# Kernel optimization log

Hardware: AMD Instinct MI355X
Metric: run time of the kernel (lower is better)

Reference implementation:

```python
import jax, jax.numpy as jnp
import numpy as np

C = 64; NET = 32; K = 3; G = 4; GC = C // G; P = K * K
STRIDE = 1; PAD = 1; DIL = 1; OFFSET_SCALE = 1.0
BN_EPS = 1e-5; LN_EPS = 1e-6


def conv2d(x, w, b, groups=1, pad=1):
    # x: (N,C,H,W), w: (O, I//groups, kh, kw)
    y = jax.lax.conv_general_dilated(
        x, w, (1, 1), [(pad, pad), (pad, pad)],
        feature_group_count=groups,
        dimension_numbers=('NCHW', 'OIHW', 'NCHW'))
    return y + b[None, :, None, None]


def dcnv3_core(x, offset, mask):
    """Faithful port of dcnv3_core_pytorch (InternImage).
    x: (N,H,W,C) channels-last; offset: (N,H,W,G*P*2); mask: (N,H,W,G*P) (softmaxed).
    grid_sample(bilinear, zeros padding, align_corners=False) done manually."""
    xp = jnp.pad(x, ((0, 0), (PAD, PAD), (PAD, PAD), (0, 0)))
    N, Hin, Win, _ = xp.shape
    Ho, Wo = offset.shape[1], offset.shape[2]
    # reference points in normalized [0,1] coords (x first, y second)
    start = (DIL * (K - 1)) // 2 + 0.5
    ref_x = (start + jnp.arange(Wo, dtype=jnp.float32) * STRIDE) / Win  # (Wo,)
    ref_y = (start + jnp.arange(Ho, dtype=jnp.float32) * STRIDE) / Hin  # (Ho,)
    ref = jnp.stack(jnp.broadcast_arrays(ref_x[None, :], ref_y[:, None]), axis=-1)  # (Ho,Wo,2)
    # dilation grid (kernel tap offsets, torch meshgrid 'ij' flatten order: w-major)
    kv = (jnp.arange(K, dtype=jnp.float32) * DIL - (DIL * (K - 1)) // 2)
    gx, gy = jnp.meshgrid(kv / Win, kv / Hin, indexing='ij')
    grid = jnp.stack([gx, gy], -1).reshape(P, 2)  # (P,2), same for every group
    # sampling locations, normalized: (N,Ho,Wo,G,P,2)
    off = offset.reshape(N, Ho, Wo, G, P, 2) * (OFFSET_SCALE / jnp.array([Win, Hin], jnp.float32))
    loc = ref[None, :, :, None, None, :] + grid[None, None, None, None, :, :] * OFFSET_SCALE + off
    # grid_sample align_corners=False: pixel = loc*size - 0.5  (since g = 2*loc-1)
    px = loc[..., 0] * Win - 0.5
    py = loc[..., 1] * Hin - 0.5
    x0 = jnp.floor(px); y0 = jnp.floor(py)
    ix0 = x0.astype(jnp.int32); iy0 = y0.astype(jnp.int32)
    wx1 = px - x0; wy1 = py - y0; wx0 = 1.0 - wx1; wy0 = 1.0 - wy1
    xg = xp.reshape(N, Hin, Win, G, GC)
    n_idx = jnp.arange(N)[:, None, None, None, None]
    g_idx = jnp.arange(G)[None, None, None, :, None]

    def sample(ix, iy):
        valid = ((ix >= 0) & (ix < Win) & (iy >= 0) & (iy < Hin)).astype(xg.dtype)
        v = xg[n_idx, jnp.clip(iy, 0, Hin - 1), jnp.clip(ix, 0, Win - 1), g_idx]  # (N,Ho,Wo,G,P,GC)
        return v * valid[..., None]

    val = (sample(ix0, iy0) * (wx0 * wy0)[..., None]
           + sample(ix0 + 1, iy0) * (wx1 * wy0)[..., None]
           + sample(ix0, iy0 + 1) * (wx0 * wy1)[..., None]
           + sample(ix0 + 1, iy0 + 1) * (wx1 * wy1)[..., None])
    out = jnp.einsum('nhwgpc,nhwgp->nhwgc', val, mask.reshape(N, Ho, Wo, G, P))
    return out.reshape(N, Ho, Wo, C)


def setup_inputs() -> dict:
    key = jax.random.key(0)
    ks = jax.random.split(key, 16)
    N, H, W = 4, 128, 128
    f = lambda k, shp, s=1.0: jax.random.normal(k, shp, jnp.float32) * s
    return {
        'input_x': f(ks[0], (N, C, H, W)),
        'input_y': f(ks[1], (N, NET, H, W)),
        'enc_w': f(ks[2], (NET, C), 0.05), 'enc_b': jnp.zeros((NET,), jnp.float32),
        'bn_g': jnp.ones((NET,), jnp.float32), 'bn_b': jnp.zeros((NET,), jnp.float32),
        'bn_m': jnp.zeros((NET,), jnp.float32), 'bn_v': jnp.ones((NET,), jnp.float32),
        'gru_wz': f(ks[3], (NET, 2 * NET, 3, 3), 0.05), 'gru_bz': jnp.zeros((NET,), jnp.float32),
        'gru_wr': f(ks[4], (NET, 2 * NET, 3, 3), 0.05), 'gru_br': jnp.zeros((NET,), jnp.float32),
        'gru_wq': f(ks[5], (NET, 2 * NET, 3, 3), 0.05), 'gru_bq': jnp.zeros((NET,), jnp.float32),
        'dw_w': f(ks[6], (C, 1, 3, 3), 0.1), 'dw_b': jnp.zeros((C,), jnp.float32),
        'ln_g': jnp.ones((C,), jnp.float32), 'ln_b': jnp.zeros((C,), jnp.float32),
        'off_w': f(ks[7], (G * P * 2, C), 0.1), 'off_b': f(ks[8], (G * P * 2,), 0.1),
        'mask_w': f(ks[9], (G * P, C), 0.1), 'mask_b': jnp.zeros((G * P,), jnp.float32),
        'inp_w': f(ks[10], (C, C), 0.1), 'inp_b': jnp.zeros((C,), jnp.float32),
        'out_w': f(ks[11], (C, C), 0.1), 'out_b': jnp.zeros((C,), jnp.float32),
    }


def reference(input_x, input_y, enc_w, enc_b, bn_g, bn_b, bn_m, bn_v,
              gru_wz, gru_bz, gru_wr, gru_br, gru_wq, gru_bq,
              dw_w, dw_b, ln_g, ln_b, off_w, off_b, mask_w, mask_b,
              inp_w, inp_b, out_w, out_b):
    N, _, H, W = input_x.shape
    # encoder: 1x1 Conv + BN(eval) + SiLU
    e = jnp.einsum('nchw,oc->nohw', input_x, enc_w) + enc_b[None, :, None, None]
    e = (e - bn_m[None, :, None, None]) * jax.lax.rsqrt(bn_v + BN_EPS)[None, :, None, None]
    e = e * bn_g[None, :, None, None] + bn_b[None, :, None, None]
    x_en = jax.nn.silu(e)
    # ConvGRU: h' = (1-z)*h + z*q
    hx = jnp.concatenate([input_y, x_en], axis=1)
    z = jax.nn.sigmoid(conv2d(hx, gru_wz, gru_bz))
    r = jax.nn.sigmoid(conv2d(hx, gru_wr, gru_br))
    q = jnp.tanh(conv2d(jnp.concatenate([r * input_y, x_en], axis=1), gru_wq, gru_bq))
    h = (1.0 - z) * input_y + z * q  # (N,NET,H,W)
    # channels-last main path
    inp = input_x.transpose(0, 2, 3, 1)  # (N,H,W,C)
    x = inp @ inp_w.T + inp_b
    # depthwise conv on gru state -> LN (channels_last) -> GELU
    y = conv2d(h, dw_w, dw_b, groups=NET).transpose(0, 2, 3, 1)  # (N,H,W,C)
    mu = y.mean(-1, keepdims=True)
    var = ((y - mu) ** 2).mean(-1, keepdims=True)
    y = (y - mu) * jax.lax.rsqrt(var + LN_EPS) * ln_g + ln_b
    y = jax.nn.gelu(y, approximate=False)
    offset = y @ off_w.T + off_b  # (N,H,W,G*P*2)
    m = y @ mask_w.T + mask_b
    m = jax.nn.softmax(m.reshape(N, H, W, G, P), axis=-1).reshape(N, H, W, G * P)
    x = dcnv3_core(x, offset, m)
    x = x @ out_w.T + out_b
    return jax.nn.silu(x.transpose(0, 3, 1, 2)), h
```

## Files before the change

### kernel.cpp

```cpp
#include <hip/hip_runtime.h>
#include <hip/hip_bf16.h>

typedef __hip_bfloat16 bf16;
typedef short short8v __attribute__((ext_vector_type(8)));
typedef short short4v __attribute__((ext_vector_type(4)));
typedef float float4v __attribute__((ext_vector_type(4)));

static __device__ __forceinline__ float b2f(bf16 v){ return __bfloat162float(v); }
static __device__ __forceinline__ bf16 f2b(float v){ return __float2bfloat16(v); }
static __device__ __forceinline__ float bu2f(unsigned short u){ return __uint_as_float(((unsigned)u) << 16); }
static __device__ __forceinline__ short f2bs(float v){ bf16 t = __float2bfloat16(v); return *(short*)&t; }

#define WT 128
#define HWT 16384

#define OFF_ENC   0
#define OFF_ENCSC 2048
#define OFF_ENCSH 2080
#define OFF_BZ    20544
#define OFF_BR    39008
#define OFF_BQ    57472
#define OFF_DWP   57504
#define OFF_DWB   58080
#define OFF_LNG   58144
#define OFF_LNB   58208
#define OFF_OMB   65184
#define OFF_WINP  65296
#define OFF_BINP  69392
#define OFF_BOUT  73552
#define NW_TOTAL  73616
#define NBF_ZR    36864
#define NBF_Q     18432
#define NBF_OM    7168
#define NBF_OUT   4096
#define NPREP     (NW_TOTAL + NBF_ZR + NBF_Q + NBF_OM + NBF_OUT)
#define NHALO     2064
#define NTOT      (NPREP + NHALO)

#define B_WZRB  294912
#define B_WQB   368640
#define B_WOMB  405504
#define B_WOUTB 419840
#define B_HXP   428544
#define B_QINP  9081344
#define B_ZBUF  17734144
#define B_XL    428544

__global__ void k_prep(
    const float* __restrict__ enc_w, const float* __restrict__ enc_b,
    const float* __restrict__ bn_g, const float* __restrict__ bn_b,
    const float* __restrict__ bn_m, const float* __restrict__ bn_v,
    const float* __restrict__ gwz, const float* __restrict__ gbz,
    const float* __restrict__ gwr, const float* __restrict__ gbr,
    const float* __restrict__ gwq, const float* __restrict__ gbq,
    const float* __restrict__ dww, const float* __restrict__ dwb,
    const float* __restrict__ lng, const float* __restrict__ lnb,
    const float* __restrict__ offw, const float* __restrict__ offb,
    const float* __restrict__ maskw, const float* __restrict__ maskb,
    const float* __restrict__ inpw, const float* __restrict__ inpb,
    const float* __restrict__ outw, const float* __restrict__ outb,
    float* __restrict__ Wp, bf16* __restrict__ wzrb, bf16* __restrict__ wqb,
    bf16* __restrict__ womb, bf16* __restrict__ woutb,
    bf16* __restrict__ hxp, bf16* __restrict__ qinp) {
  int i = blockIdx.x * blockDim.x + threadIdx.x;
  if (i >= NTOT) return;
  if (i >= NPREP) {
    int t = i - NPREP;
    int img = t / 516, r = t % 516;
    int ph, pw;
    if (r < 130) { ph = 0; pw = r; }
    else if (r < 260) { ph = 129; pw = r - 130; }
    else if (r < 388) { ph = r - 260 + 1; pw = 0; }
    else { ph = r - 388 + 1; pw = 129; }
    size_t pb = (((size_t)img * 130 + ph) * 130 + pw) * 64;
    uint4 zz = make_uint4(0, 0, 0, 0);
    #pragma unroll
    for (int k = 0; k < 8; ++k) {
      ((uint4*)(hxp + pb))[k] = zz;
      ((uint4*)(qinp + pb))[k] = zz;
    }
    return;
  }
  if (i >= NW_TOTAL) {
    int d = i - NW_TOTAL;
    if (d < NBF_ZR) {
      int n = d / 576, k = d % 576;
      int tap = k >> 6, cin = k & 63;
      float v = (n < 32) ? gwz[(n*64 + cin)*9 + tap] : gwr[((n-32)*64 + cin)*9 + tap];
      wzrb[d] = f2b(v);
    } else if (d < NBF_ZR + NBF_Q) {
      int d2 = d - NBF_ZR;
      int n = d2 / 576, k = d2 % 576;
      int tap = k >> 6, cin = k & 63;
      wqb[d2] = f2b(gwq[(n*64 + cin)*9 + tap]);
    } else if (d < NBF_ZR + NBF_Q + NBF_OM) {
      int d3 = d - NBF_ZR - NBF_Q;
      int j = d3 >> 6, c = d3 & 63;
      float v = (j < 72) ? offw[j*64 + c] : ((j < 108) ? maskw[(j-72)*64 + c] : 0.f);
      womb[d3] = f2b(v);
    } else {
      int d4 = d - NBF_ZR - NBF_Q - NBF_OM;
      int o = d4 >> 6, c = d4 & 63;
      woutb[d4] = f2b(outw[o*64 + c]);
    }
    return;
  }
  float v;
  if (i < 2048) { int c = i >> 5, o = i & 31; v = enc_w[o*64 + c]; }
  else if (i < 2080) { int o = i - 2048; v = bn_g[o] * rsqrtf(bn_v[o] + 1e-5f); }
  else if (i < 2112) { int o = i - 2080;
    float sc = bn_g[o] * rsqrtf(bn_v[o] + 1e-5f);
    v = (enc_b[o] - bn_m[o]) * sc + bn_b[o]; }
  else if (i < 20544) { v = 0.f; }
  else if (i < 20576) { v = gbz[i - OFF_BZ]; }
  else if (i < 39008) { v = 0.f; }
  else if (i < 39040) { v = gbr[i - OFF_BR]; }
  else if (i < 57472) { v = 0.f; }
  else if (i < 57504) { v = gbq[i - OFF_BQ]; }
  else if (i < 58080) { int d = i - OFF_DWP; int tap = d >> 6, o = d & 63; v = dww[o*9 + tap]; }
  else if (i < 58144) { v = dwb[i - OFF_DWB]; }
  else if (i < 58208) { v = lng[i - OFF_LNG]; }
  else if (i < 58272) { v = lnb[i - OFF_LNB]; }
  else if (i < 65184) { v = 0.f; }
  else if (i < 65292) { int j = i - OFF_OMB; v = (j < 72) ? offb[j] : maskb[j-72]; }
  else if (i < 65296) { v = 0.f; }
  else if (i < 69392) { int d = i - OFF_WINP; int c = d >> 6, o = d & 63; v = inpw[o*64 + c]; }
  else if (i < 69456) { v = inpb[i - OFF_BINP]; }
  else if (i < 73552) { v = 0.f; }
  else { v = outb[i - OFF_BOUT]; }
  Wp[i] = v;
}

__global__ void __launch_bounds__(256) k_pre(
    const float* __restrict__ X, const float* __restrict__ Y,
    const float* __restrict__ Wp, bf16* __restrict__ hxp, bf16* __restrict__ qinp) {
  __shared__ float xls[4096];
  int tid = threadIdx.x;
  int px = tid & 63, sect = tid >> 6;
  int img = blockIdx.z, h = blockIdx.y, w0 = blockIdx.x * 64;
  int hw = h * WT + w0 + px;
  const float* xp = X + (size_t)img * (64 * HWT) + hw;
  #pragma unroll
  for (int i = 0; i < 16; ++i) {
    int c = sect * 16 + i;
    xls[c * 64 + px] = xp[c * HWT];
  }
  const float* yp = Y + (size_t)img * (32 * HWT) + hw;
  bf16 yv[8];
  #pragma unroll
  for (int i = 0; i < 8; ++i) yv[i] = f2b(yp[(sect * 8 + i) * HWT]);
  size_t pb = (((size_t)img * 130 + h + 1) * 130 + (w0 + px + 1)) * 64;
  *(uint4*)(hxp + pb + sect * 8) = *(const uint4*)yv;
  __syncthreads();
  float aen[8];
  #pragma unroll
  for (int o = 0; o < 8; ++o) aen[o] = 0.f;
  for (int k = 0; k < 64; ++k) {
    float a = xls[k * 64 + px];
    const float* we = Wp + OFF_ENC + k * 32 + sect * 8;
    #pragma unroll
    for (int o = 0; o < 8; ++o) aen[o] += a * we[o];
  }
  bf16 xe[8];
  #pragma unroll
  for (int o = 0; o < 8; ++o) {
    int oo = sect * 8 + o;
    float e = aen[o] * Wp[OFF_ENCSC + oo] + Wp[OFF_ENCSH + oo];
    xe[o] = f2b(e / (1.f + __expf(-e)));
  }
  *(uint4*)(hxp + pb + 32 + sect * 8) = *(const uint4*)xe;
  *(uint4*)(qinp + pb + 32 + sect * 8) = *(const uint4*)xe;
}

__global__ void __launch_bounds__(256) k_zr(
    const float* __restrict__ Wp,
    const bf16* __restrict__ hxp, const bf16* __restrict__ wzrb,
    bf16* __restrict__ qinp, bf16* __restrict__ zbuf) {
  __shared__ short zt[32 * 132];
  int tid = threadIdx.x;
  int wv = tid >> 6, ln = tid & 63;
  int quad = ln >> 4, lm = ln & 15;
  int img = blockIdx.z, h = blockIdx.y;
  int p0 = wv * 32;
  const short* hs = (const short*)hxp;
  const short* ws = (const short*)wzrb;
  size_t rowb = ((size_t)img * 130 + h + 1) * 130;
  const short* ab0 = hs + (rowb + p0 + lm + 1) * 64 + quad * 8;
  const short* ab1 = ab0 + 16 * 64;
  int bb = lm * 576 + quad * 8;
  float4v acc[8];
  #pragma unroll
  for (int t = 0; t < 8; ++t) acc[t] = (float4v){0.f, 0.f, 0.f, 0.f};
  #pragma unroll
  for (int kc = 0; kc < 18; ++kc) {
    const int tap = kc >> 1, cin0 = (kc & 1) * 32;
    const int dd = (tap / 3 - 1) * 130 + (tap % 3 - 1);
    short8v a0 = *(const short8v*)(ab0 + dd * 64 + cin0);
    short8v a1 = *(const short8v*)(ab1 + dd * 64 + cin0);
    #pragma unroll
    for (int t = 0; t < 4; ++t) {
      short8v b = *(const short8v*)(ws + bb + t * (16 * 576) + kc * 32);
      acc[t*2]   = __builtin_amdgcn_mfma_f32_16x16x32_bf16(a0, b, acc[t*2], 0, 0, 0);
      acc[t*2+1] = __builtin_amdgcn_mfma_f32_16x16x32_bf16(a1, b, acc[t*2+1], 0, 0, 0);
    }
  }
  #pragma unroll
  for (int mt = 0; mt < 2; ++mt) {
    #pragma unroll
    for (int t = 0; t < 2; ++t) {
      int n = t * 16 + lm;
      float bz = Wp[OFF_BZ + n];
      short zp[4];
      #pragma unroll
      for (int ri = 0; ri < 4; ++ri)
        zp[ri] = f2bs(1.f / (1.f + __expf(-(acc[t*2+mt][ri] + bz))));
      *(short4v*)(zt + n * 132 + p0 + mt * 16 + quad * 4) = *(const short4v*)zp;
    }
  }
  #pragma unroll
  for (int mt = 0; mt < 2; ++mt) {
    #pragma unroll
    for (int t = 2; t < 4; ++t) {
      int c = (t - 2) * 16 + lm;
      float br = Wp[OFF_BR + c];
      #pragma unroll
      for (int ri = 0; ri < 4; ++ri) {
        int px = p0 + mt * 16 + quad * 4 + ri;
        size_t aoff = (rowb + px + 1) * 64 + c;
        float rv = 1.f / (1.f + __expf(-(acc[t*2+mt][ri] + br)));
        float yv = b2f(hxp[aoff]);
        qinp[aoff] = f2b(rv * yv);
      }
    }
  }
  __syncthreads();
  int n2 = tid >> 3, pq = tid & 7;
  short8v z0 = *(const short8v*)(zt + n2 * 132 + pq * 16);
  short8v z1 = *(const short8v*)(zt + n2 * 132 + pq * 16 + 8);
  short* zo = (short*)zbuf + (((size_t)img * 128 + h) * 32 + n2) * 128 + pq * 16;
  *(short8v*)zo = z0;
  *(short8v*)(zo + 8) = z1;
}

__global__ void __launch_bounds__(256) k_qg(
    const float* __restrict__ Y, const float* __restrict__ Wp,
    const bf16* __restrict__ qinp, const bf16* __restrict__ wqb,
    const bf16* __restrict__ zbuf, float* __restrict__ outh) {
  __shared__ float hout[32 * 132];
  int tid = threadIdx.x;
  int wv = tid >> 6, ln = tid & 63;
  int quad = ln >> 4, lm = ln & 15;
  int img = blockIdx.z, h = blockIdx.y;
  int p0 = wv * 32;
  const short* qs = (const short*)qinp;
  const short* ws = (const short*)wqb;
  size_t rowb = ((size_t)img * 130 + h + 1) * 130;
  const short* ab0 = qs + (rowb + p0 + lm + 1) * 64 + quad * 8;
  const short* ab1 = ab0 + 16 * 64;
  int bb = lm * 576 + quad * 8;
  float4v acc[4];
  #pragma unroll
  for (int t = 0; t < 4; ++t) acc[t] = (float4v){0.f, 0.f, 0.f, 0.f};
  #pragma unroll
  for (int kc = 0; kc < 18; ++kc) {
    const int tap = kc >> 1, cin0 = (kc & 1) * 32;
    const int dd = (tap / 3 - 1) * 130 + (tap % 3 - 1);
    short8v a0 = *(const short8v*)(ab0 + dd * 64 + cin0);
    short8v a1 = *(const short8v*)(ab1 + dd * 64 + cin0);
    #pragma unroll
    for (int t = 0; t < 2; ++t) {
      short8v b = *(const short8v*)(ws + bb + t * (16 * 576) + kc * 32);
      acc[t*2]   = __builtin_amdgcn_mfma_f32_16x16x32_bf16(a0, b, acc[t*2], 0, 0, 0);
      acc[t*2+1] = __builtin_amdgcn_mfma_f32_16x16x32_bf16(a1, b, acc[t*2+1], 0, 0, 0);
    }
  }
  #pragma unroll
  for (int mt = 0; mt < 2; ++mt) {
    #pragma unroll
    for (int t = 0; t < 2; ++t) {
      int n = t * 16 + lm;
      float bq = Wp[OFF_BQ + n];
      float4 hv;
      hv.x = acc[t*2+mt][0] + bq; hv.y = acc[t*2+mt][1] + bq;
      hv.z = acc[t*2+mt][2] + bq; hv.w = acc[t*2+mt][3] + bq;
      *(float4*)(hout + n * 132 + p0 + mt * 16 + quad * 4) = hv;
    }
  }
  __syncthreads();
  const short* zbb = (const short*)zbuf + ((size_t)img * 128 + h) * 32 * 128;
  #pragma unroll
  for (int r = 0; r < 4; ++r) {
    int n = (tid >> 5) + r * 8;
    int px4 = (tid & 31) * 4;
    float4 hv = *(const float4*)(hout + n * 132 + px4);
    uint2 zz = *(const uint2*)(zbb + n * 128 + px4);
    size_t gb = ((size_t)img * 32 + n) * HWT + h * 128 + px4;
    float4 yv = *(const float4*)(Y + gb);
    float z0 = bu2f((unsigned short)(zz.x & 0xFFFFu)), z1 = bu2f((unsigned short)(zz.x >> 16));
    float z2 = bu2f((unsigned short)(zz.y & 0xFFFFu)), z3 = bu2f((unsigned short)(zz.y >> 16));
    float4 o;
    o.x = (1.f - z0) * yv.x + z0 * tanhf(hv.x);
    o.y = (1.f - z1) * yv.y + z1 * tanhf(hv.y);
    o.z = (1.f - z2) * yv.z + z2 * tanhf(hv.z);
    o.w = (1.f - z3) * yv.w + z3 * tanhf(hv.w);
    *(float4*)(outh + gb) = o;
  }
}

__global__ void __launch_bounds__(256) k_xl(
    const float* __restrict__ X, const float* __restrict__ Wp, bf16* __restrict__ xl) {
  __shared__ float xls[4096];
  int tid = threadIdx.x;
  int px = tid & 63, sect = tid >> 6;
  int img = blockIdx.z, h = blockIdx.y, w0 = blockIdx.x * 64;
  int hw = h * WT + w0 + px;
  const float* xp = X + (size_t)img * (64 * HWT) + hw;
  #pragma unroll
  for (int i = 0; i < 16; ++i) {
    int c = sect * 16 + i;
    xls[c * 64 + px] = xp[c * HWT];
  }
  __syncthreads();
  float acc[16];
  #pragma unroll
  for (int o = 0; o < 16; ++o) acc[o] = Wp[OFF_BINP + sect * 16 + o];
  for (int k = 0; k < 64; ++k) {
    float a = xls[k * 64 + px];
    const float* wr = Wp + OFF_WINP + k * 64 + sect * 16;
    #pragma unroll
    for (int o = 0; o < 16; ++o) acc[o] += a * wr[o];
  }
  bf16 ov[16];
  #pragma unroll
  for (int o = 0; o < 16; ++o) ov[o] = f2b(acc[o]);
  bf16* op = xl + ((size_t)img * HWT + hw) * 64 + sect * 16;
  ((uint4*)op)[0] = ((const uint4*)ov)[0];
  ((uint4*)op)[1] = ((const uint4*)ov)[1];
}

#define LDS_PSA  0
#define LDS_PSB  2048
#define LDS_STAT 4096
#define LDS_Y    4608
#define LDS_OM   13824
#define LDS_TOT  42752

__global__ void __launch_bounds__(512) k_mega(
    const float* __restrict__ Wp, const float* __restrict__ hb,
    const bf16* __restrict__ xl, const bf16* __restrict__ womb,
    const bf16* __restrict__ woutb, float* __restrict__ out0) {
  __shared__ char smem[LDS_TOT];
  float* psa  = (float*)(smem + LDS_PSA);
  float* psb  = (float*)(smem + LDS_PSB);
  float* stat = (float*)(smem + LDS_STAT);
  short* yls  = (short*)(smem + LDS_Y);
  float* omls = (float*)(smem + LDS_OM);
  short* vls  = (short*)(smem + LDS_Y);

  int tid = threadIdx.x;
  int img = blockIdx.z, h = blockIdx.y, w0 = blockIdx.x * 64;

  int wloc = tid & 63, part = tid >> 6;
  int w = w0 + wloc;
  float yv[8];
  {
    const float* hn = hb + (size_t)img * (32 * HWT);
    #pragma unroll
    for (int i = 0; i < 8; ++i) yv[i] = Wp[OFF_DWB + part*8 + i];
    #pragma unroll
    for (int tap = 0; tap < 9; ++tap) {
      int dy = tap / 3 - 1, dx = tap % 3 - 1;
      int hh = h + dy, ww = w + dx;
      bool ok = ((unsigned)hh < 128u) && ((unsigned)ww < 128u);
      int off = hh * WT + ww;
      #pragma unroll
      for (int j = 0; j < 4; ++j) {
        int cin = part * 4 + j;
        float a = ok ? hn[cin * HWT + off] : 0.f;
        yv[2*j]   += a * Wp[OFF_DWP + tap*64 + part*8 + 2*j];
        yv[2*j+1] += a * Wp[OFF_DWP + tap*64 + part*8 + 2*j+1];
      }
    }
  }
  float lsum = 0.f, lsq = 0.f;
  #pragma unroll
  for (int i = 0; i < 8; ++i) { lsum += yv[i]; lsq += yv[i]*yv[i]; }
  psa[part * 64 + wloc] = lsum;
  psb[part * 64 + wloc] = lsq;
  __syncthreads();
  if (tid < 64) {
    float s = 0.f, q = 0.f;
    #pragma unroll
    for (int p = 0; p < 8; ++p) { s += psa[p*64 + tid]; q += psb[p*64 + tid]; }
    float mu = s * (1.f/64.f);
    float var = q * (1.f/64.f) - mu * mu;
    stat[tid*2] = mu;
    stat[tid*2+1] = rsqrtf(var + 1e-6f);
  }
  __syncthreads();
  {
    float mu = stat[wloc*2], inv = stat[wloc*2+1];
    bf16 tmp[8];
    #pragma unroll
    for (int i = 0; i < 8; ++i) {
      int c = part*8 + i;
      float v = (yv[i] - mu) * inv * Wp[OFF_LNG + c] + Wp[OFF_LNB + c];
      tmp[i] = f2b(0.5f * v * (1.f + erff(v * 0.70710678118654752f)));
    }
    *(short8v*)(yls + wloc*72 + part*8) = *(const short8v*)tmp;
  }
  __syncthreads();

  int wv = tid >> 6, ln = tid & 63, quad = ln >> 4, lm = ln & 15;
  if (wv < 7) {
    const short* wb = (const short*)womb;
    float4v acc[4];
    #pragma unroll
    for (int mt = 0; mt < 4; ++mt) acc[mt] = (float4v){0.f,0.f,0.f,0.f};
    #pragma unroll
    for (int kc = 0; kc < 2; ++kc) {
      short8v b = *(const short8v*)(wb + (wv*16 + lm)*64 + kc*32 + quad*8);
      #pragma unroll
      for (int mt = 0; mt < 4; ++mt) {
        short8v a = *(const short8v*)(yls + (mt*16 + lm)*72 + kc*32 + quad*8);
        acc[mt] = __builtin_amdgcn_mfma_f32_16x16x32_bf16(a, b, acc[mt], 0, 0, 0);
      }
    }
    float bias = Wp[OFF_OMB + wv*16 + lm];
    #pragma unroll
    for (int mt = 0; mt < 4; ++mt) {
      #pragma unroll
      for (int ri = 0; ri < 4; ++ri)
        omls[(mt*16 + quad*4 + ri)*113 + wv*16 + lm] = acc[mt][ri] + bias;
    }
  }
  __syncthreads();

  {
    int px = tid >> 3, g = (tid >> 1) & 3, half = tid & 1;
    const float* oml = omls + px*113;
    float m[9];
    #pragma unroll
    for (int p = 0; p < 9; ++p) m[p] = oml[72 + g*9 + p];
    float mx = m[0];
    #pragma unroll
    for (int p = 1; p < 9; ++p) mx = fmaxf(mx, m[p]);
    float sum = 0.f;
    #pragma unroll
    for (int p = 0; p < 9; ++p) { m[p] = __expf(m[p] - mx); sum += m[p]; }
    float rs = 1.f / sum;
    int wg = w0 + px;
    const bf16* xn = xl + (size_t)img * (HWT * 64);
    float acc[8];
    #pragma unroll
    for (int i = 0; i < 8; ++i) acc[i] = 0.f;
    for (int p = 0; p < 9; ++p) {
      float bx = (float)(wg + p / 3 - 1);
      float by = (float)(h + p % 3 - 1);
      float ox = oml[g*18 + p*2];
      float oy = oml[g*18 + p*2 + 1];
      float mk = m[p] * rs;
      float pxx = bx + ox, pyy = by + oy;
      float fx = floorf(pxx), fy = floorf(pyy);
      int jx0 = (int)fx, jy0 = (int)fy;
      float wx1 = pxx - fx, wy1 = pyy - fy;
      float wx0 = 1.f - wx1, wy0 = 1.f - wy1;
      int cjx[4] = { jx0, jx0 + 1, jx0, jx0 + 1 };
      int cjy[4] = { jy0, jy0, jy0 + 1, jy0 + 1 };
      float cw[4] = { wx0*wy0, wx1*wy0, wx0*wy1, wx1*wy1 };
      #pragma unroll
      for (int k = 0; k < 4; ++k) {
        if ((unsigned)cjx[k] < 128u && (unsigned)cjy[k] < 128u) {
          float cf = mk * cw[k];
          const bf16* s = xn + (size_t)(cjy[k] * WT + cjx[k]) * 64 + g * 16 + half * 8;
          uint4 u0 = *(const uint4*)(s);
          const unsigned uu[4] = {u0.x,u0.y,u0.z,u0.w};
          #pragma unroll
          for (int q = 0; q < 4; ++q) {
            acc[2*q]     += cf * bu2f((unsigned short)(uu[q] & 0xFFFFu));
            acc[2*q + 1] += cf * bu2f((unsigned short)(uu[q] >> 16));
          }
        }
      }
    }
    bf16 tmp[8];
    #pragma unroll
    for (int i = 0; i < 8; ++i) tmp[i] = f2b(acc[i]);
    *(short8v*)(vls + px*72 + g*16 + half*8) = *(const short8v*)tmp;
  }
  __syncthreads();

  if (wv < 4) {
    const short* wb = (const short*)woutb;
    float4v acc[4];
    #pragma unroll
    for (int mt = 0; mt < 4; ++mt) acc[mt] = (float4v){0.f,0.f,0.f,0.f};
    #pragma unroll
    for (int kc = 0; kc < 2; ++kc) {
      short8v b = *(const short8v*)(wb + (wv*16 + lm)*64 + kc*32 + quad*8);
      #pragma unroll
      for (int mt = 0; mt < 4; ++mt) {
        short8v a = *(const short8v*)(vls + (mt*16 + lm)*72 + kc*32 + quad*8);
        acc[mt] = __builtin_amdgcn_mfma_f32_16x16x32_bf16(a, b, acc[mt], 0, 0, 0);
      }
    }
    int ch = wv*16 + lm;
    float bias = Wp[OFF_BOUT + ch];
    #pragma unroll
    for (int mt = 0; mt < 4; ++mt) {
      float4 v;
      float s0 = acc[mt][0] + bias; v.x = s0 / (1.f + __expf(-s0));
      float s1 = acc[mt][1] + bias; v.y = s1 / (1.f + __expf(-s1));
      float s2 = acc[mt][2] + bias; v.z = s2 / (1.f + __expf(-s2));
      float s3 = acc[mt][3] + bias; v.w = s3 / (1.f + __expf(-s3));
      *(float4*)(out0 + ((size_t)img*64 + ch)*HWT + h*128 + w0 + mt*16 + quad*4) = v;
    }
  }
}

extern "C" void kernel_launch(void* const* d_in, const int* in_sizes, int n_in,
                              void* d_out, int out_size, void* d_ws, size_t ws_size,
                              hipStream_t stream) {
  const float* input_x = (const float*)d_in[0];
  const float* input_y = (const float*)d_in[1];

  float* Wp = (float*)d_ws;
  bf16* WZRB  = (bf16*)((char*)d_ws + B_WZRB);
  bf16* WQB   = (bf16*)((char*)d_ws + B_WQB);
  bf16* WOMB  = (bf16*)((char*)d_ws + B_WOMB);
  bf16* WOUTB = (bf16*)((char*)d_ws + B_WOUTB);
  bf16* HXP   = (bf16*)((char*)d_ws + B_HXP);
  bf16* QINP  = (bf16*)((char*)d_ws + B_QINP);
  bf16* ZBUF  = (bf16*)((char*)d_ws + B_ZBUF);
  bf16* XL    = (bf16*)((char*)d_ws + B_XL);
  float* out0 = (float*)d_out;
  float* outh = (float*)d_out + 4194304;

  k_prep<<<dim3((NTOT + 255)/256), dim3(256), 0, stream>>>(
      (const float*)d_in[2], (const float*)d_in[3], (const float*)d_in[4], (const float*)d_in[5],
      (const float*)d_in[6], (const float*)d_in[7], (const float*)d_in[8], (const float*)d_in[9],
      (const float*)d_in[10], (const float*)d_in[11], (const float*)d_in[12], (const float*)d_in[13],
      (const float*)d_in[14], (const float*)d_in[15], (const float*)d_in[16], (const float*)d_in[17],
      (const float*)d_in[18], (const float*)d_in[19], (const float*)d_in[20], (const float*)d_in[21],
      (const float*)d_in[22], (const float*)d_in[23], (const float*)d_in[24], (const float*)d_in[25],
      Wp, WZRB, WQB, WOMB, WOUTB, HXP, QINP);
  k_pre<<<dim3(2, 128, 4), dim3(256), 0, stream>>>(input_x, input_y, Wp, HXP, QINP);
  k_zr <<<dim3(1, 128, 4), dim3(256), 0, stream>>>(Wp, HXP, WZRB, QINP, ZBUF);
  k_qg <<<dim3(1, 128, 4), dim3(256), 0, stream>>>(input_y, Wp, QINP, WQB, ZBUF, outh);
  k_xl <<<dim3(2, 128, 4), dim3(256), 0, stream>>>(input_x, Wp, XL);
  k_mega<<<dim3(2, 128, 4), dim3(512), 0, stream>>>(Wp, outh, XL, WOMB, WOUTB, out0);
}
```

Baseline: 271.6 us.

## Fuse input projection into k_pre and stage r*y writes through LDS

The separate k_xl kernel, which reloaded input_x and computed the input linear projection, is removed. That projection is now computed in k_pre alongside the encoder conv, reusing the x tile already in LDS, and XL moves to its own workspace region so it no longer aliases HXP. In k_zr the scattered per-element bf16 writes of r*y into qinp now go into an LDS tile first and are written out as 16-byte vectors. The trade-offs are one fewer launch and one fewer read of input_x, against higher register pressure in k_pre from 16 extra accumulators and extra LDS in k_zr.

Measured after the change: 275.2 us. About the same (+1.3%).

```diff
diff --git a/kernel.cpp b/kernel.cpp
--- a/kernel.cpp
+++ b/kernel.cpp
@@ -44,7 +44,7 @@
 #define B_HXP   428544
 #define B_QINP  9081344
 #define B_ZBUF  17734144
-#define B_XL    428544
+#define B_XL    21928448
 
 __global__ void k_prep(
     const float* __restrict__ enc_w, const float* __restrict__ enc_b,
@@ -133,7 +133,8 @@
 
 __global__ void __launch_bounds__(256) k_pre(
     const float* __restrict__ X, const float* __restrict__ Y,
-    const float* __restrict__ Wp, bf16* __restrict__ hxp, bf16* __restrict__ qinp) {
+    const float* __restrict__ Wp, bf16* __restrict__ hxp, bf16* __restrict__ qinp,
+    bf16* __restrict__ xl) {
   __shared__ float xls[4096];
   int tid = threadIdx.x;
   int px = tid & 63, sect = tid >> 6;
@@ -152,14 +153,19 @@
   size_t pb = (((size_t)img * 130 + h + 1) * 130 + (w0 + px + 1)) * 64;
   *(uint4*)(hxp + pb + sect * 8) = *(const uint4*)yv;
   __syncthreads();
-  float aen[8];
+  float aen[8], axl[16];
   #pragma unroll
   for (int o = 0; o < 8; ++o) aen[o] = 0.f;
+  #pragma unroll
+  for (int o = 0; o < 16; ++o) axl[o] = Wp[OFF_BINP + sect * 16 + o];
   for (int k = 0; k < 64; ++k) {
     float a = xls[k * 64 + px];
     const float* we = Wp + OFF_ENC + k * 32 + sect * 8;
+    const float* wr = Wp + OFF_WINP + k * 64 + sect * 16;
     #pragma unroll
     for (int o = 0; o < 8; ++o) aen[o] += a * we[o];
+    #pragma unroll
+    for (int o = 0; o < 16; ++o) axl[o] += a * wr[o];
   }
   bf16 xe[8];
   #pragma unroll
@@ -170,6 +176,12 @@
   }
   *(uint4*)(hxp + pb + 32 + sect * 8) = *(const uint4*)xe;
   *(uint4*)(qinp + pb + 32 + sect * 8) = *(const uint4*)xe;
+  bf16 ov[16];
+  #pragma unroll
+  for (int o = 0; o < 16; ++o) ov[o] = f2b(axl[o]);
+  bf16* op = xl + ((size_t)img * HWT + hw) * 64 + sect * 16;
+  ((uint4*)op)[0] = ((const uint4*)ov)[0];
+  ((uint4*)op)[1] = ((const uint4*)ov)[1];
 }
 
 __global__ void __launch_bounds__(256) k_zr(
@@ -177,6 +189,7 @@
     const bf16* __restrict__ hxp, const bf16* __restrict__ wzrb,
     bf16* __restrict__ qinp, bf16* __restrict__ zbuf) {
   __shared__ short zt[32 * 132];
+  __shared__ short ryt[128 * 40];
   int tid = threadIdx.x;
   int wv = tid >> 6, ln = tid & 63;
   int quad = ln >> 4, lm = ln & 15;
@@ -226,20 +239,29 @@
       #pragma unroll
       for (int ri = 0; ri < 4; ++ri) {
         int px = p0 + mt * 16 + quad * 4 + ri;
-        size_t aoff = (rowb + px + 1) * 64 + c;
         float rv = 1.f / (1.f + __expf(-(acc[t*2+mt][ri] + br)));
-        float yv = b2f(hxp[aoff]);
-        qinp[aoff] = f2b(rv * yv);
+        float yy = b2f(hxp[(rowb + px + 1) * 64 + c]);
+        ryt[px * 40 + c] = f2bs(rv * yy);
       }
     }
   }
   __syncthreads();
-  int n2 = tid >> 3, pq = tid & 7;
-  short8v z0 = *(const short8v*)(zt + n2 * 132 + pq * 16);
-  short8v z1 = *(const short8v*)(zt + n2 * 132 + pq * 16 + 8);
-  short* zo = (short*)zbuf + (((size_t)img * 128 + h) * 32 + n2) * 128 + pq * 16;
-  *(short8v*)zo = z0;
-  *(short8v*)(zo + 8) = z1;
+  {
+    int n2 = tid >> 3, pq = tid & 7;
+    short8v z0 = *(const short8v*)(zt + n2 * 132 + pq * 16);
+    short8v z1 = *(const short8v*)(zt + n2 * 132 + pq * 16 + 8);
+    short* zo = (short*)zbuf + (((size_t)img * 128 + h) * 32 + n2) * 128 + pq * 16;
+    *(short8v*)zo = z0;
+    *(short8v*)(zo + 8) = z1;
+  }
+  {
+    int px = tid >> 1, chalf = tid & 1;
+    short8v r0 = *(const short8v*)(ryt + px * 40 + chalf * 16);
+    short8v r1 = *(const short8v*)(ryt + px * 40 + chalf * 16 + 8);
+    short* qo = (short*)qinp + (rowb + px + 1) * 64 + chalf * 16;
+    *(short8v*)qo = r0;
+    *(short8v*)(qo + 8) = r1;
+  }
 }
 
 __global__ void __launch_bounds__(256) k_qg(
@@ -307,37 +329,6 @@
   }
 }
 
-__global__ void __launch_bounds__(256) k_xl(
-    const float* __restrict__ X, const float* __restrict__ Wp, bf16* __restrict__ xl) {
-  __shared__ float xls[4096];
-  int tid = threadIdx.x;
-  int px = tid & 63, sect = tid >> 6;
-  int img = blockIdx.z, h = blockIdx.y, w0 = blockIdx.x * 64;
-  int hw = h * WT + w0 + px;
-  const float* xp = X + (size_t)img * (64 * HWT) + hw;
-  #pragma unroll
-  for (int i = 0; i < 16; ++i) {
-    int c = sect * 16 + i;
-    xls[c * 64 + px] = xp[c * HWT];
-  }
-  __syncthreads();
-  float acc[16];
-  #pragma unroll
-  for (int o = 0; o < 16; ++o) acc[o] = Wp[OFF_BINP + sect * 16 + o];
-  for (int k = 0; k < 64; ++k) {
-    float a = xls[k * 64 + px];
-    const float* wr = Wp + OFF_WINP + k * 64 + sect * 16;
-    #pragma unroll
-    for (int o = 0; o < 16; ++o) acc[o] += a * wr[o];
-  }
-  bf16 ov[16];
-  #pragma unroll
-  for (int o = 0; o < 16; ++o) ov[o] = f2b(acc[o]);
-  bf16* op = xl + ((size_t)img * HWT + hw) * 64 + sect * 16;
-  ((uint4*)op)[0] = ((const uint4*)ov)[0];
-  ((uint4*)op)[1] = ((const uint4*)ov)[1];
-}
-
 #define LDS_PSA  0
 #define LDS_PSB  2048
 #define LDS_STAT 4096
@@ -544,9 +535,8 @@
       (const float*)d_in[18], (const float*)d_in[19], (const float*)d_in[20], (const float*)d_in[21],
       (const float*)d_in[22], (const float*)d_in[23], (const float*)d_in[24], (const float*)d_in[25],
       Wp, WZRB, WQB, WOMB, WOUTB, HXP, QINP);
-  k_pre<<<dim3(2, 128, 4), dim3(256), 0, stream>>>(input_x, input_y, Wp, HXP, QINP);
+  k_pre<<<dim3(2, 128, 4), dim3(256), 0, stream>>>(input_x, input_y, Wp, HXP, QINP, XL);
   k_zr <<<dim3(1, 128, 4), dim3(256), 0, stream>>>(Wp, HXP, WZRB, QINP, ZBUF);
   k_qg <<<dim3(1, 128, 4), dim3(256), 0, stream>>>(input_y, Wp, QINP, WQB, ZBUF, outh);
-  k_xl <<<dim3(2, 128, 4), dim3(256), 0, stream>>>(input_x, Wp, XL);
   k_mega<<<dim3(2, 128, 4), dim3(512), 0, stream>>>(Wp, outh, XL, WOMB, WOUTB, out0);
 }
```
